# Kernel optimization log

Measured on AMD Instinct MI355X. Metric: run time of the kernel, lower is better.

The kernel has to match this reference:

```python
import jax, jax.numpy as jnp
import numpy as np
import math

N, I, C, T, V, M = 256, 2, 6, 300, 25, 2
D = 256
IN_DIM = I * C * T * V * M  # 180000


def _const_mats():
    a = math.radians(30.0)
    ca, sa = math.cos(a), math.sin(a)
    R_x = np.array([[1, 0, 0], [0, ca, sa], [0, -sa, ca]], np.float32).T
    R_y = np.array([[ca, 0, -sa], [0, 1, 0], [sa, 0, ca]], np.float32).T
    R_z = np.array([[ca, sa, 0], [-sa, ca, 0], [0, 0, 1]], np.float32).T
    R_rotate = R_x @ R_y @ R_z
    R_scale = np.diag([2.0, 2.0, 2.0]).astype(np.float32)
    R_shear = np.ones((3, 3), np.float32)  # sh_next=1 -> all ones (transpose is identity op)
    return R_rotate, R_shear, R_scale


def _param_mats():
    rotate_w = np.zeros((3, 3), np.float32)
    rotate_w[0, 0] = 1.0
    rotate_w[1, 1] = rotate_w[1, 2] = rotate_w[2, 1] = rotate_w[2, 2] = 0.7
    shear_w = np.full((3, 3), 0.8, np.float32)
    np.fill_diagonal(shear_w, 1.0)
    scale_w = np.diag([0.6, 0.6, 0.6]).astype(np.float32)
    return rotate_w, shear_w, scale_w


def setup_inputs() -> dict:
    key = jax.random.key(0)
    k1, k2 = jax.random.split(key)
    R_rotate, R_shear, R_scale = _const_mats()
    rotate_w, shear_w, scale_w = _param_mats()
    x = jax.random.normal(k1, (N, I, C, T, V, M), jnp.float32)
    W = jax.random.normal(k2, (IN_DIM, D), jnp.float32) * (1.0 / math.sqrt(IN_DIM))
    b = jnp.zeros((D,), jnp.float32)
    return {
        "x": x,
        "rotate_weight": jnp.asarray(rotate_w),
        "shear_weight": jnp.asarray(shear_w),
        "scale_weight": jnp.asarray(scale_w),
        "W_backbone": W,
        "b_backbone": b,
        "R_rotate": jnp.asarray(R_rotate),
        "R_shear": jnp.asarray(R_shear),
        "R_scale": jnp.asarray(R_scale),
    }


def _loss_fn(q, z, n):
    q = q / jnp.linalg.norm(q, axis=-1, keepdims=True)
    z = z / jnp.linalg.norm(z, axis=-1, keepdims=True)
    sim = q @ z.T                       # [N, N]
    diag = jnp.diagonal(sim)            # (q*z).sum(-1)
    offdiag_sum = sim.sum(axis=-1) - diag
    return diag - offdiag_sum / (n - 1)


def reference(x, rotate_weight, shear_weight, scale_weight, W_backbone, b_backbone,
              R_rotate, R_shear, R_scale):
    n, i, c, t, v, m = x.shape
    # per-pass effective 3x3 matrices (elementwise gated constants)
    Rr = R_rotate * rotate_weight
    Rs = R_shear * shear_weight
    Rc = R_scale * scale_weight
    Rtot = Rr @ Rs @ Rc  # sequential passes compose: y @ Rr @ Rs @ Rc
    # split C=6 into two xyz chunks, rotate coord axis (vectorized over N,I,chunk,T,V,M)
    xr = x.reshape(n, i, 2, 3, t, v, m)
    x_aug = jnp.einsum("nhctvm,cd->nhdtvm", xr.reshape(n * i, 2 * 0 + 2, 3, t, v, m)[0:0] if False else xr.reshape(n, i * 2, 3, t, v, m), Rtot)
    x_aug = x_aug.reshape(n, i, c, t, v, m)
    # torch x1 = x aliases: x2 == x1 == augmented tensor -> both branches identical
    feats = x_aug.reshape(n, -1)
    z = feats @ W_backbone + b_backbone  # backbone; projector(num_layers=0) is identity
    out = z                              # out1 == out2 == z
    q = z                                # predictor is identity
    z_d = jax.lax.stop_gradient(z)
    loss = _loss_fn(q, z_d, n) + _loss_fn(q, z_d, n)
    return (loss.mean(), out, out)
```

## Files before the change

kernel.cpp:

```cpp
#include <hip/hip_runtime.h>

typedef __attribute__((ext_vector_type(4))) short bf16x4;
typedef __attribute__((ext_vector_type(8))) short bf16x8;
typedef __attribute__((ext_vector_type(16))) float f32x16;
typedef __attribute__((ext_vector_type(4))) float f32x4;
typedef __attribute__((ext_vector_type(4))) unsigned int u32x4;

__device__ __forceinline__ unsigned short f2bf(float f) {
    unsigned int u = __builtin_bit_cast(unsigned int, f);
    u += 0x7fffu + ((u >> 16) & 1u);
    return (unsigned short)(u >> 16);
}

#define PA 196

#define ISSUE(RW, kb, sub) do { \
    _Pragma("unroll") \
    for (int jj_ = 0; jj_ < 2; ++jj_) { \
        const int vk2_ = jj_*8 + (tid >> 6); \
        const int vk_  = (sub)*32 + vk2_*2; \
        const int c3_  = vk_ >> 6, pl_ = vk_ & 63; \
        f32x4 q0_ = {0.f,0.f,0.f,0.f}, q1_ = {0.f,0.f,0.f,0.f}; \
        if (pl_ < 60) { \
            const float* wr_ = W + ((kb) + (long)c3_*15000 + pl_)*256 + (tid & 63)*4; \
            q0_ = *(const f32x4*)wr_; \
            q1_ = *(const f32x4*)(wr_ + 256); \
        } \
        RW[jj_*8+0]=q0_.x; RW[jj_*8+1]=q0_.y; RW[jj_*8+2]=q0_.z; RW[jj_*8+3]=q0_.w; \
        RW[jj_*8+4]=q1_.x; RW[jj_*8+5]=q1_.y; RW[jj_*8+6]=q1_.z; RW[jj_*8+7]=q1_.w; \
    } \
} while (0)

#define PACK(RW, bufsel) do { \
    _Pragma("unroll") \
    for (int jj_ = 0; jj_ < 2; ++jj_) { \
        const int vk2_ = jj_*8 + (tid >> 6); \
        u32x4 pw_; \
        pw_.x = (unsigned)f2bf(RW[jj_*8+0]) | ((unsigned)f2bf(RW[jj_*8+4]) << 16); \
        pw_.y = (unsigned)f2bf(RW[jj_*8+1]) | ((unsigned)f2bf(RW[jj_*8+5]) << 16); \
        pw_.z = (unsigned)f2bf(RW[jj_*8+2]) | ((unsigned)f2bf(RW[jj_*8+6]) << 16); \
        pw_.w = (unsigned)f2bf(RW[jj_*8+3]) | ((unsigned)f2bf(RW[jj_*8+7]) << 16); \
        *((u32x4*)&lds_b[bufsel][vk2_*256 + (tid & 63)*4]) = pw_; \
    } \
} while (0)

#define ASTAGE(kb) do { \
    const float* xs_ = x + (kb); \
    _Pragma("unroll 2") \
    for (int k_ = 0; k_ < 8; ++k_) { \
        const int it_ = k_*512 + tid; \
        if (it_ < 3840) { \
            const int n_  = (int)(((unsigned)it_ * 4370u) >> 16);   \
            const int pl_ = (it_ - n_*15) * 4; \
            const float* px_ = xs_ + (long)n_*180000 + pl_; \
            const f32x4 c0_ = *(const f32x4*)px_; \
            const f32x4 c1_ = *(const f32x4*)(px_ + 15000); \
            const f32x4 c2_ = *(const f32x4*)(px_ + 30000); \
            bf16x4 o0_, o1_, o2_; \
            _Pragma("unroll") \
            for (int e_ = 0; e_ < 4; ++e_) { \
                o0_[e_] = (short)f2bf(c0_[e_]*RT[0] + c1_[e_]*RT[3] + c2_[e_]*RT[6]); \
                o1_[e_] = (short)f2bf(c0_[e_]*RT[1] + c1_[e_]*RT[4] + c2_[e_]*RT[7]); \
                o2_[e_] = (short)f2bf(c0_[e_]*RT[2] + c1_[e_]*RT[5] + c2_[e_]*RT[8]); \
            } \
            const int a_ = n_*PA + pl_; \
            *(bf16x4*)&lds_a[a_      ] = o0_; \
            *(bf16x4*)&lds_a[a_ +  64] = o1_; \
            *(bf16x4*)&lds_a[a_ + 128] = o2_; \
        } \
    } \
} while (0)

#define MFMASTEP(jstep) do { \
    const unsigned int* bb_ = lds_b[(jstep) & 1]; \
    _Pragma("unroll") \
    for (int kk_ = 0; kk_ < 2; ++kk_) { \
        const int kb_ = (jstep)*32 + kk_*16 + lh*8; \
        bf16x8 af_[2]; \
        _Pragma("unroll") \
        for (int fm_ = 0; fm_ < 2; ++fm_) { \
            const unsigned short* pa_ = &lds_a[(m0 + fm_*32 + lm)*PA + kb_]; \
            bf16x4 alo_ = *(const bf16x4*)pa_; \
            bf16x4 ahi_ = *(const bf16x4*)(pa_ + 4); \
            af_[fm_] = __builtin_shufflevector(alo_, ahi_, 0,1,2,3,4,5,6,7); \
        } \
        _Pragma("unroll") \
        for (int fd_ = 0; fd_ < 4; ++fd_) { \
            const int db_ = d0 + fd_*32 + lm; \
            const int v2_ = kk_*8 + lh*4; \
            u32x4 bw_ = { bb_[(v2_+0)*256 + db_], bb_[(v2_+1)*256 + db_], \
                          bb_[(v2_+2)*256 + db_], bb_[(v2_+3)*256 + db_] }; \
            bf16x8 bv_ = __builtin_bit_cast(bf16x8, bw_); \
            _Pragma("unroll") \
            for (int fm_ = 0; fm_ < 2; ++fm_) \
                acc[fm_][fd_] = __builtin_amdgcn_mfma_f32_32x32x16_bf16(af_[fm_], bv_, acc[fm_][fd_], 0, 0, 0); \
        } \
    } \
} while (0)

__global__ __launch_bounds__(512, 2) void gemm_kernel(
    const float* __restrict__ x,
    const float* __restrict__ rw, const float* __restrict__ sw, const float* __restrict__ cw,
    const float* __restrict__ W,
    const float* __restrict__ Rr, const float* __restrict__ Rs, const float* __restrict__ Rc,
    float* __restrict__ P)
{
    __shared__ unsigned short lds_a[256 * PA];
    __shared__ unsigned int   lds_b[2][16 * 256];

    const int tid = threadIdx.x;
    const int blk = blockIdx.x;
    const int p0 = blk * 60;

    float Ar[9], Br[9], Cr[9], T1[9], RT[9];
    #pragma unroll
    for (int e = 0; e < 9; ++e) {
        Ar[e] = Rr[e] * rw[e];
        Br[e] = Rs[e] * sw[e];
        Cr[e] = Rc[e] * cw[e];
    }
    #pragma unroll
    for (int r = 0; r < 3; ++r)
        #pragma unroll
        for (int c = 0; c < 3; ++c)
            T1[r*3+c] = Ar[r*3+0]*Br[0*3+c] + Ar[r*3+1]*Br[1*3+c] + Ar[r*3+2]*Br[2*3+c];
    #pragma unroll
    for (int r = 0; r < 3; ++r)
        #pragma unroll
        for (int c = 0; c < 3; ++c)
            RT[r*3+c] = T1[r*3+0]*Cr[0*3+c] + T1[r*3+1]*Cr[1*3+c] + T1[r*3+2]*Cr[2*3+c];

    if (tid < 256) {
        bf16x4 zz = (bf16x4)0;
        #pragma unroll
        for (int c3 = 0; c3 < 3; ++c3)
            *((bf16x4*)&lds_a[tid*PA + c3*64 + 60]) = zz;
    }

    const int w  = tid >> 6, l = tid & 63;
    const int lm = l & 31,  lh = l >> 5;
    const int m0 = (w >> 1) * 64;
    const int d0 = (w & 1) * 128;

    f32x16 acc[2][4];
    #pragma unroll
    for (int fm = 0; fm < 2; ++fm)
        #pragma unroll
        for (int fd = 0; fd < 4; ++fd)
            acc[fm][fd] = (f32x16)0.0f;

    float RWa[16], RWb[16];

    ISSUE(RWa, (long)p0, 0);
    ASTAGE((long)p0);
    ISSUE(RWb, (long)p0, 1);
    PACK(RWa, 0);
    __syncthreads();

    for (int slab = 0; slab < 4; ++slab) {
        const long kbase = (long)slab * 45000 + p0;
        const long kbnxt = kbase + 45000;
        #pragma unroll
        for (int j = 0; j < 6; ++j) {
            if (j < 4) {
                if (j & 1) ISSUE(RWb, kbase, j+2);
                else       ISSUE(RWa, kbase, j+2);
            } else if (slab < 3) {
                if (j & 1) ISSUE(RWb, kbnxt, j-4);
                else       ISSUE(RWa, kbnxt, j-4);
            }
            if (j == 0 && slab > 0) {
                ASTAGE(kbase);
                __syncthreads();
            }
            MFMASTEP(j);
            if (j < 5) {
                if (j & 1) PACK(RWa, ((j+1)&1));
                else       PACK(RWb, ((j+1)&1));
            } else if (slab < 3) {
                PACK(RWa, 0);
            }
            __syncthreads();
        }
    }

    float* Pb = P + (size_t)blk * 65536;
    #pragma unroll
    for (int fm = 0; fm < 2; ++fm)
        #pragma unroll
        for (int fd = 0; fd < 4; ++fd)
            #pragma unroll
            for (int r = 0; r < 16; ++r) {
                int row = m0 + fm*32 + (r & 3) + 8*(r >> 2) + 4*lh;
                int col = d0 + fd*32 + lm;
                Pb[row*256 + col] = acc[fm][fd][r];
            }
}

__global__ __launch_bounds__(1024) void reduce_kernel(
    const float* __restrict__ P, const float* __restrict__ bias,
    float* __restrict__ out, float* __restrict__ Z)
{
    __shared__ float sred[4][256];
    __shared__ float wsum[16];
    const int n = blockIdx.x;
    const int tid = threadIdx.x;
    const int sg = tid >> 8, d = tid & 255;

    const float* p = P + (size_t)n*256 + d;
    float z = 0.f;
    #pragma unroll 8
    for (int s = sg; s < 250; s += 4) z += p[(size_t)s * 65536];
    sred[sg][d] = z;
    __syncthreads();

    float zf = 0.f;
    if (sg == 0) zf = sred[0][d] + sred[1][d] + sred[2][d] + sred[3][d] + bias[d];
    float sq = zf * zf;
    #pragma unroll
    for (int off = 32; off > 0; off >>= 1) sq += __shfl_down(sq, off, 64);
    if ((tid & 63) == 0) wsum[tid >> 6] = sq;
    __syncthreads();
    if (sg == 0) {
        float tot = wsum[0] + wsum[1] + wsum[2] + wsum[3];
        float inv = rsqrtf(tot);
        out[1 + n*256 + d]         = zf;
        out[1 + 65536 + n*256 + d] = zf;
        Z[n*256 + d] = zf * inv;
    }
}

__global__ __launch_bounds__(1024) void loss_kernel(const float* __restrict__ Z, float* __restrict__ out)
{
    __shared__ float sp[4][256];
    __shared__ float w4[16];
    const int tid = threadIdx.x;
    const int g = tid >> 8, d = tid & 255;
    float S = 0.f;
    #pragma unroll 8
    for (int n = g*64; n < g*64 + 64; ++n) S += Z[n*256 + d];
    sp[g][d] = S;
    __syncthreads();
    float v = 0.f;
    if (g == 0) {
        S = sp[0][d] + sp[1][d] + sp[2][d] + sp[3][d];
        v = S * S;
    }
    #pragma unroll
    for (int off = 32; off > 0; off >>= 1) v += __shfl_down(v, off, 64);
    if ((tid & 63) == 0) w4[tid >> 6] = v;
    __syncthreads();
    if (tid == 0) {
        float tot = w4[0] + w4[1] + w4[2] + w4[3];
        out[0] = 2.0f - (2.0f / 255.0f) * (tot * (1.0f / 256.0f) - 1.0f);
    }
}

extern "C" void kernel_launch(void* const* d_in, const int* in_sizes, int n_in,
                              void* d_out, int out_size, void* d_ws, size_t ws_size,
                              hipStream_t stream)
{
    (void)in_sizes; (void)n_in; (void)out_size; (void)ws_size;
    const float* x  = (const float*)d_in[0];
    const float* rw = (const float*)d_in[1];
    const float* sw = (const float*)d_in[2];
    const float* cw = (const float*)d_in[3];
    const float* W  = (const float*)d_in[4];
    const float* bb = (const float*)d_in[5];
    const float* Rr = (const float*)d_in[6];
    const float* Rs = (const float*)d_in[7];
    const float* Rc = (const float*)d_in[8];
    float* out = (float*)d_out;
    float* P = (float*)d_ws;
    float* Z = P + (size_t)250 * 65536;

    gemm_kernel<<<250, 512, 0, stream>>>(x, rw, sw, cw, W, Rr, Rs, Rc, P);
    reduce_kernel<<<256, 1024, 0, stream>>>(P, bb, out, Z);
    loss_kernel<<<1, 1024, 0, stream>>>(Z, out);
}
```

Before: 412.1 us.

## Repartition GEMM K-dimension into per-output-channel chunks of 200 positions

Reworks the split-K GEMM so each block processes four chunks of 200 contiguous positions of a single output channel. Each chunk loads the three input xyz channels and applies one column of the 3x3 transform. Before, each block handled 60 positions with all three output channels across four slabs. K steps shrink to 16 per MFMA step, giving 52 pipelined steps and a smaller LDS B buffer. The grid drops from 250 to 225 blocks so partial sums fit one wave of CUs and the reduce reads fewer partials. The cost is that x is reloaded three times per chunk group, once per output channel, instead of being reused across three channels.

```diff
diff --git a/kernel.cpp b/kernel.cpp
--- a/kernel.cpp
+++ b/kernel.cpp
@@ -12,89 +12,77 @@
     return (unsigned short)(u >> 16);
 }
 
-#define PA 196
-
-#define ISSUE(RW, kb, sub) do { \
+#define PA 212
+
+__device__ __forceinline__ void chunk_params(int ch, long& KB, long& XB, int& d) {
+    int i_ = ch / 450, r_ = ch - 450 * i_;
+    int c_ = r_ / 75,  pc_ = r_ - 75 * c_;
+    KB = (long)(i_ * 6 + c_) * 15000 + pc_ * 200;
+    XB = (long)i_ * 90000 + (c_ >= 3 ? 45000 : 0) + pc_ * 200;
+    d  = c_ - (c_ >= 3 ? 3 : 0);
+}
+
+#define ISSUE(R, KB, SUB) do { \
+    const int vk2_ = tid >> 6; \
+    const int pl_  = (SUB)*16 + vk2_*2; \
+    f32x4 q0_ = {0.f,0.f,0.f,0.f}, q1_ = {0.f,0.f,0.f,0.f}; \
+    if (pl_ < 200) { \
+        const float* wr_ = W + ((KB) + (long)pl_)*256 + (tid & 63)*4; \
+        q0_ = *(const f32x4*)wr_; \
+        q1_ = *(const f32x4*)(wr_ + 256); \
+    } \
+    R[0]=q0_.x; R[1]=q0_.y; R[2]=q0_.z; R[3]=q0_.w; \
+    R[4]=q1_.x; R[5]=q1_.y; R[6]=q1_.z; R[7]=q1_.w; \
+} while (0)
+
+#define PACK(R, BUF) do { \
+    u32x4 pw_; \
+    pw_.x = (unsigned)f2bf(R[0]) | ((unsigned)f2bf(R[4]) << 16); \
+    pw_.y = (unsigned)f2bf(R[1]) | ((unsigned)f2bf(R[5]) << 16); \
+    pw_.z = (unsigned)f2bf(R[2]) | ((unsigned)f2bf(R[6]) << 16); \
+    pw_.w = (unsigned)f2bf(R[3]) | ((unsigned)f2bf(R[7]) << 16); \
+    *((u32x4*)&lds_b[BUF][(tid >> 6)*256 + (tid & 63)*4]) = pw_; \
+} while (0)
+
+#define ASTAGE(XB, A0, A1, A2) do { \
+    _Pragma("unroll 5") \
+    for (int k_ = 0; k_ < 25; ++k_) { \
+        const int it_ = k_*512 + tid; \
+        const int n_  = (int)(((unsigned)it_ * 5243u) >> 18);   \
+        const int q_  = it_ - n_*50; \
+        const float* px_ = x + (long)n_*180000 + (XB) + q_*4; \
+        const f32x4 c0_ = *(const f32x4*)px_; \
+        const f32x4 c1_ = *(const f32x4*)(px_ + 15000); \
+        const f32x4 c2_ = *(const f32x4*)(px_ + 30000); \
+        bf16x4 o_; \
+        _Pragma("unroll") \
+        for (int e_ = 0; e_ < 4; ++e_) \
+            o_[e_] = (short)f2bf(c0_[e_]*(A0) + c1_[e_]*(A1) + c2_[e_]*(A2)); \
+        *(bf16x4*)&lds_a[n_*PA + q_*4] = o_; \
+    } \
+} while (0)
+
+#define MFMASTEP(J, BUFSEL) do { \
+    const unsigned int* bb_ = lds_b[BUFSEL]; \
+    const int kb_ = (J)*16 + lh*8; \
+    bf16x8 af_[2]; \
     _Pragma("unroll") \
-    for (int jj_ = 0; jj_ < 2; ++jj_) { \
-        const int vk2_ = jj_*8 + (tid >> 6); \
-        const int vk_  = (sub)*32 + vk2_*2; \
-        const int c3_  = vk_ >> 6, pl_ = vk_ & 63; \
-        f32x4 q0_ = {0.f,0.f,0.f,0.f}, q1_ = {0.f,0.f,0.f,0.f}; \
-        if (pl_ < 60) { \
-            const float* wr_ = W + ((kb) + (long)c3_*15000 + pl_)*256 + (tid & 63)*4; \
-            q0_ = *(const f32x4*)wr_; \
-            q1_ = *(const f32x4*)(wr_ + 256); \
-        } \
-        RW[jj_*8+0]=q0_.x; RW[jj_*8+1]=q0_.y; RW[jj_*8+2]=q0_.z; RW[jj_*8+3]=q0_.w; \
-        RW[jj_*8+4]=q1_.x; RW[jj_*8+5]=q1_.y; RW[jj_*8+6]=q1_.z; RW[jj_*8+7]=q1_.w; \
-    } \
-} while (0)
-
-#define PACK(RW, bufsel) do { \
+    for (int fm_ = 0; fm_ < 2; ++fm_) { \
+        const unsigned short* pa_ = &lds_a[(m0 + fm_*32 + lm)*PA + kb_]; \
+        bf16x4 alo_ = *(const bf16x4*)pa_; \
+        bf16x4 ahi_ = *(const bf16x4*)(pa_ + 4); \
+        af_[fm_] = __builtin_shufflevector(alo_, ahi_, 0,1,2,3,4,5,6,7); \
+    } \
     _Pragma("unroll") \
-    for (int jj_ = 0; jj_ < 2; ++jj_) { \
-        const int vk2_ = jj_*8 + (tid >> 6); \
-        u32x4 pw_; \
-        pw_.x = (unsigned)f2bf(RW[jj_*8+0]) | ((unsigned)f2bf(RW[jj_*8+4]) << 16); \
-        pw_.y = (unsigned)f2bf(RW[jj_*8+1]) | ((unsigned)f2bf(RW[jj_*8+5]) << 16); \
-        pw_.z = (unsigned)f2bf(RW[jj_*8+2]) | ((unsigned)f2bf(RW[jj_*8+6]) << 16); \
-        pw_.w = (unsigned)f2bf(RW[jj_*8+3]) | ((unsigned)f2bf(RW[jj_*8+7]) << 16); \
-        *((u32x4*)&lds_b[bufsel][vk2_*256 + (tid & 63)*4]) = pw_; \
-    } \
-} while (0)
-
-#define ASTAGE(kb) do { \
-    const float* xs_ = x + (kb); \
-    _Pragma("unroll 2") \
-    for (int k_ = 0; k_ < 8; ++k_) { \
-        const int it_ = k_*512 + tid; \
-        if (it_ < 3840) { \
-            const int n_  = (int)(((unsigned)it_ * 4370u) >> 16);   \
-            const int pl_ = (it_ - n_*15) * 4; \
-            const float* px_ = xs_ + (long)n_*180000 + pl_; \
-            const f32x4 c0_ = *(const f32x4*)px_; \
-            const f32x4 c1_ = *(const f32x4*)(px_ + 15000); \
-            const f32x4 c2_ = *(const f32x4*)(px_ + 30000); \
-            bf16x4 o0_, o1_, o2_; \
-            _Pragma("unroll") \
-            for (int e_ = 0; e_ < 4; ++e_) { \
-                o0_[e_] = (short)f2bf(c0_[e_]*RT[0] + c1_[e_]*RT[3] + c2_[e_]*RT[6]); \
-                o1_[e_] = (short)f2bf(c0_[e_]*RT[1] + c1_[e_]*RT[4] + c2_[e_]*RT[7]); \
-                o2_[e_] = (short)f2bf(c0_[e_]*RT[2] + c1_[e_]*RT[5] + c2_[e_]*RT[8]); \
-            } \
-            const int a_ = n_*PA + pl_; \
-            *(bf16x4*)&lds_a[a_      ] = o0_; \
-            *(bf16x4*)&lds_a[a_ +  64] = o1_; \
-            *(bf16x4*)&lds_a[a_ + 128] = o2_; \
-        } \
-    } \
-} while (0)
-
-#define MFMASTEP(jstep) do { \
-    const unsigned int* bb_ = lds_b[(jstep) & 1]; \
-    _Pragma("unroll") \
-    for (int kk_ = 0; kk_ < 2; ++kk_) { \
-        const int kb_ = (jstep)*32 + kk_*16 + lh*8; \
-        bf16x8 af_[2]; \
+    for (int fd_ = 0; fd_ < 4; ++fd_) { \
+        const int db_ = d0 + fd_*32 + lm; \
+        const int v2_ = lh*4; \
+        u32x4 bw_ = { bb_[(v2_+0)*256 + db_], bb_[(v2_+1)*256 + db_], \
+                      bb_[(v2_+2)*256 + db_], bb_[(v2_+3)*256 + db_] }; \
+        bf16x8 bv_ = __builtin_bit_cast(bf16x8, bw_); \
         _Pragma("unroll") \
-        for (int fm_ = 0; fm_ < 2; ++fm_) { \
-            const unsigned short* pa_ = &lds_a[(m0 + fm_*32 + lm)*PA + kb_]; \
-            bf16x4 alo_ = *(const bf16x4*)pa_; \
-            bf16x4 ahi_ = *(const bf16x4*)(pa_ + 4); \
-            af_[fm_] = __builtin_shufflevector(alo_, ahi_, 0,1,2,3,4,5,6,7); \
-        } \
-        _Pragma("unroll") \
-        for (int fd_ = 0; fd_ < 4; ++fd_) { \
-            const int db_ = d0 + fd_*32 + lm; \
-            const int v2_ = kk_*8 + lh*4; \
-            u32x4 bw_ = { bb_[(v2_+0)*256 + db_], bb_[(v2_+1)*256 + db_], \
-                          bb_[(v2_+2)*256 + db_], bb_[(v2_+3)*256 + db_] }; \
-            bf16x8 bv_ = __builtin_bit_cast(bf16x8, bw_); \
-            _Pragma("unroll") \
-            for (int fm_ = 0; fm_ < 2; ++fm_) \
-                acc[fm_][fd_] = __builtin_amdgcn_mfma_f32_32x32x16_bf16(af_[fm_], bv_, acc[fm_][fd_], 0, 0, 0); \
-        } \
+        for (int fm_ = 0; fm_ < 2; ++fm_) \
+            acc[fm_][fd_] = __builtin_amdgcn_mfma_f32_32x32x16_bf16(af_[fm_], bv_, acc[fm_][fd_], 0, 0, 0); \
     } \
 } while (0)
 
@@ -106,11 +94,10 @@
     float* __restrict__ P)
 {
     __shared__ unsigned short lds_a[256 * PA];
-    __shared__ unsigned int   lds_b[2][16 * 256];
+    __shared__ unsigned int   lds_b[2][8 * 256];
 
     const int tid = threadIdx.x;
     const int blk = blockIdx.x;
-    const int p0 = blk * 60;
 
     float Ar[9], Br[9], Cr[9], T1[9], RT[9];
     #pragma unroll
@@ -132,9 +119,8 @@
 
     if (tid < 256) {
         bf16x4 zz = (bf16x4)0;
-        #pragma unroll
-        for (int c3 = 0; c3 < 3; ++c3)
-            *((bf16x4*)&lds_a[tid*PA + c3*64 + 60]) = zz;
+        *((bf16x4*)&lds_a[tid*PA + 200]) = zz;
+        *((bf16x4*)&lds_a[tid*PA + 204]) = zz;
     }
 
     const int w  = tid >> 6, l = tid & 63;
@@ -149,36 +135,39 @@
         for (int fd = 0; fd < 4; ++fd)
             acc[fm][fd] = (f32x16)0.0f;
 
-    float RWa[16], RWb[16];
-
-    ISSUE(RWa, (long)p0, 0);
-    ASTAGE((long)p0);
-    ISSUE(RWb, (long)p0, 1);
-    PACK(RWa, 0);
-    __syncthreads();
-
-    for (int slab = 0; slab < 4; ++slab) {
-        const long kbase = (long)slab * 45000 + p0;
-        const long kbnxt = kbase + 45000;
-        #pragma unroll
-        for (int j = 0; j < 6; ++j) {
-            if (j < 4) {
-                if (j & 1) ISSUE(RWb, kbase, j+2);
-                else       ISSUE(RWa, kbase, j+2);
-            } else if (slab < 3) {
-                if (j & 1) ISSUE(RWb, kbnxt, j-4);
-                else       ISSUE(RWa, kbnxt, j-4);
-            }
-            if (j == 0 && slab > 0) {
-                ASTAGE(kbase);
+    float RW0[8], RW1[8];
+
+    {
+        long KB0, XB0; int dd0;
+        chunk_params(4*blk, KB0, XB0, dd0);
+        ISSUE(RW0, KB0, 0);
+        ASTAGE(XB0, RT[dd0], RT[3+dd0], RT[6+dd0]);
+        ISSUE(RW1, KB0, 1);
+        PACK(RW0, 0);
+    }
+    __syncthreads();
+
+    for (int cc = 0; cc < 4; ++cc) {
+        long KB, XB; int dd;
+        chunk_params(4*blk + cc, KB, XB, dd);
+        for (int j = 0; j < 13; ++j) {
+            const int u = cc*13 + j;
+            if (u + 2 < 52) {
+                const int u2 = u + 2;
+                const int cc2 = u2 / 13, j2 = u2 - 13*cc2;
+                long KB2, XB2; int dd2;
+                chunk_params(4*blk + cc2, KB2, XB2, dd2);
+                if (u & 1) ISSUE(RW1, KB2, j2);
+                else       ISSUE(RW0, KB2, j2);
+            }
+            if (j == 0 && cc > 0) {
+                ASTAGE(XB, RT[dd], RT[3+dd], RT[6+dd]);
                 __syncthreads();
             }
-            MFMASTEP(j);
-            if (j < 5) {
-                if (j & 1) PACK(RWa, ((j+1)&1));
-                else       PACK(RWb, ((j+1)&1));
-            } else if (slab < 3) {
-                PACK(RWa, 0);
+            MFMASTEP(j, (u & 1));
+            if (u < 51) {
+                if (u & 1) PACK(RW0, ((u+1) & 1));
+                else       PACK(RW1, ((u+1) & 1));
             }
             __syncthreads();
         }
@@ -210,7 +199,7 @@
     const float* p = P + (size_t)n*256 + d;
     float z = 0.f;
     #pragma unroll 8
-    for (int s = sg; s < 250; s += 4) z += p[(size_t)s * 65536];
+    for (int s = sg; s < 225; s += 4) z += p[(size_t)s * 65536];
     sred[sg][d] = z;
     __syncthreads();
 
@@ -272,9 +261,9 @@
     const float* Rc = (const float*)d_in[8];
     float* out = (float*)d_out;
     float* P = (float*)d_ws;
-    float* Z = P + (size_t)250 * 65536;
-
-    gemm_kernel<<<250, 512, 0, stream>>>(x, rw, sw, cw, W, Rr, Rs, Rc, P);
+    float* Z = P + (size_t)225 * 65536;
+
+    gemm_kernel<<<225, 512, 0, stream>>>(x, rw, sw, cw, W, Rr, Rs, Rc, P);
     reduce_kernel<<<256, 1024, 0, stream>>>(P, bb, out, Z);
     loss_kernel<<<1, 1024, 0, stream>>>(Z, out);
 }
```

Measured after the change: 468.1 us. 1.14x slower.
